# Kernel optimization log

Hardware: AMD Instinct MI355X
Metric: run time of the kernel (lower is better)

## Reference

```python
import jax, jax.numpy as jnp
import numpy as np

N, C_IN, C_OUT, K_CHEB, BATCH = 2048, 64, 64, 4, 8


def setup_inputs() -> dict:
    key = jax.random.key(0)
    k1, k2, k3, k4, k5 = jax.random.split(key, 5)
    # Xavier-uniform-like scales
    s_nn = float(np.sqrt(6.0 / (N + N)))
    s_th = float(np.sqrt(6.0 / (C_IN + C_OUT)))
    return {
        "X": jax.random.normal(k1, (BATCH, N, C_IN), dtype=jnp.float32),
        "Ws": jax.random.uniform(k2, (N, N), jnp.float32, -s_nn, s_nn),
        "W_alpha": jax.random.uniform(k3, (N, N), jnp.float32, -s_nn, s_nn),
        "Theta_s": jax.random.uniform(k4, (K_CHEB, C_IN, C_OUT), jnp.float32, -s_th, s_th),
        "Theta_d": jax.random.uniform(k5, (K_CHEB, C_IN, C_OUT), jnp.float32, -s_th, s_th),
    }


def reference(X, Ws, W_alpha, Theta_s, Theta_d):
    B, n, c_in = X.shape
    K = Theta_s.shape[0]

    # ---- static filter: sum_k (T_k(Ws) @ X) @ Theta_s[k] ----
    # T_0 = I, so T_0 @ X = X
    static_filter = jnp.einsum('bni,io->bno', X, Theta_s[0])
    if K > 1:
        T_prev2 = jnp.eye(n, dtype=X.dtype)
        T_prev1 = Ws  # T_1
        for k in range(1, K):
            TkX = jnp.einsum('nm,bmi->bni', T_prev1, X)
            static_filter = static_filter + jnp.einsum('bni,io->bno', TkX, Theta_s[k])
            if k + 1 < K:  # incremental Chebyshev recursion (same values as from-scratch)
                T_prev2, T_prev1 = T_prev1, 2.0 * (Ws @ T_prev1) - T_prev2

    # ---- dynamic filter ----
    # Wd = X @ (W_alpha @ X)^T  -> [B, n, n]
    WaX = jnp.einsum('nm,bmi->bni', W_alpha, X)
    Wd = jnp.einsum('bni,bmi->bnm', X, WaX)

    dynamic_filter = jnp.einsum('bni,io->bno', X, Theta_d[0])
    if K > 1:
        Td_prev2 = jnp.broadcast_to(jnp.eye(n, dtype=X.dtype), (B, n, n))
        Td_prev1 = Wd  # T_1
        for k in range(1, K):
            TkX = jnp.einsum('bnm,bmi->bni', Td_prev1, X)
            dynamic_filter = dynamic_filter + jnp.einsum('bni,io->bno', TkX, Theta_d[k])
            if k + 1 < K:
                Td_prev2, Td_prev1 = Td_prev1, 2.0 * jnp.matmul(Wd, Td_prev1) - Td_prev2

    return jax.nn.relu(static_filter) + jax.nn.relu(dynamic_filter)
```

## Files before the change

kernel.cpp:

```cpp
#include <hip/hip_runtime.h>

typedef __attribute__((ext_vector_type(8))) short bf16x8;
typedef __attribute__((ext_vector_type(4))) float f32x4;

__device__ __forceinline__ ushort f32_to_bf16(float f) {
    union { float f; unsigned u; } v; v.f = f;
    unsigned b = v.u + 0x7FFF + ((v.u >> 16) & 1);
    return (ushort)(b >> 16);
}
__device__ __forceinline__ float bf16_to_f32(ushort h) {
    union { unsigned u; float f; } v; v.u = ((unsigned)h) << 16;
    return v.f;
}
__device__ __forceinline__ void split2(float x, ushort& a, ushort& b) {
    a = f32_to_bf16(x); float r1 = x - bf16_to_f32(a);
    b = f32_to_bf16(r1);
}

__device__ __forceinline__ void vmwait4() { asm volatile("s_waitcnt vmcnt(4)" ::: "memory"); }
__device__ __forceinline__ void vmwait0() { asm volatile("s_waitcnt vmcnt(0)" ::: "memory"); }
__device__ __forceinline__ void lgwait0() { asm volatile("s_waitcnt lgkmcnt(0)" ::: "memory"); }
__device__ __forceinline__ void blockbar() {
    __builtin_amdgcn_sched_barrier(0);
    __builtin_amdgcn_s_barrier();
    __builtin_amdgcn_sched_barrier(0);
}

__device__ __forceinline__ void stage64x64(const ushort* gsrc, int row_stride_elems,
                                           char* lds, int t256) {
    const char* gb = (const char*)gsrc;
    const int rs = row_stride_elems * 2;
#pragma unroll
    for (int j = 0; j < 2; ++j) {
        int o = (j * 256 + t256) * 16;
        int row = o >> 7;
        int col = (o & 127) ^ ((row & 7) << 4);
        __builtin_amdgcn_global_load_lds(
            (const __attribute__((address_space(1))) unsigned int*)(gb + row * rs + col),
            (__attribute__((address_space(3))) unsigned int*)(lds + o), 16, 0, 0);
    }
}

__device__ __forceinline__ bf16x8 fragld(const char* lds, int row, int kbyte) {
    return *(const bf16x8*)(lds + (row << 7) + (kbyte ^ ((row & 7) << 4)));
}

__global__ __launch_bounds__(256) void prep_all(const float* __restrict__ X,
        ushort* __restrict__ XT1, ushort* __restrict__ XT2,
        ushort* __restrict__ X1o, ushort* __restrict__ X2o,
        const float* __restrict__ Ws, ushort* __restrict__ Ws16,
        const float* __restrict__ Wa, ushort* __restrict__ Wa1, ushort* __restrict__ Wa2,
        const float* __restrict__ Ths, ushort* __restrict__ ThsT) {
    __shared__ float tile[64][68];
    const int bx = blockIdx.x;
    const int t = threadIdx.x;
    if (bx < 256) {
        const int b = bx >> 5, n0 = (bx & 31) * 64;
#pragma unroll
        for (int it = 0; it < 4; ++it) {
            int f = it * 256 + t, r = f >> 4, q = (f & 15) * 4;
            float4 v = *(const float4*)&X[((size_t)b * 2048 + n0 + r) * 64 + q];
            tile[r][q + 0] = v.x; tile[r][q + 1] = v.y; tile[r][q + 2] = v.z; tile[r][q + 3] = v.w;
        }
        __syncthreads();
#pragma unroll
        for (int it = 0; it < 4; ++it) {
            int f = it * 256 + t, c = f >> 4, q = (f & 15) * 4;
            ushort4 h1, h2;
            split2(tile[q + 0][c], h1.x, h2.x); split2(tile[q + 1][c], h1.y, h2.y);
            split2(tile[q + 2][c], h1.z, h2.z); split2(tile[q + 3][c], h1.w, h2.w);
            size_t a = (size_t)(b * 64 + c) * 2048 + n0 + q;
            *(ushort4*)&XT1[a] = h1; *(ushort4*)&XT2[a] = h2;
        }
#pragma unroll
        for (int it = 0; it < 4; ++it) {
            int f = it * 256 + t, n = f >> 4, q = (f & 15) * 4;
            ushort4 h1, h2;
            split2(tile[n][q + 0], h1.x, h2.x); split2(tile[n][q + 1], h1.y, h2.y);
            split2(tile[n][q + 2], h1.z, h2.z); split2(tile[n][q + 3], h1.w, h2.w);
            size_t a = (size_t)(n0 + n) * 512 + b * 64 + q;
            *(ushort4*)&X1o[a] = h1; *(ushort4*)&X2o[a] = h2;
        }
    } else if (bx < 2304) {
        size_t idx = ((size_t)(bx - 256) * 256 + t) * 8;
#pragma unroll
        for (int h = 0; h < 2; ++h) {
            float4 v = *(const float4*)&Ws[idx + h * 4];
            ushort4 a;
            a.x = f32_to_bf16(v.x); a.y = f32_to_bf16(v.y);
            a.z = f32_to_bf16(v.z); a.w = f32_to_bf16(v.w);
            *(ushort4*)&Ws16[idx + h * 4] = a;
        }
    } else if (bx < 4352) {
        size_t idx = ((size_t)(bx - 2304) * 256 + t) * 8;
#pragma unroll
        for (int h = 0; h < 2; ++h) {
            float4 v = *(const float4*)&Wa[idx + h * 4];
            ushort4 a, b;
            split2(v.x, a.x, b.x); split2(v.y, a.y, b.y);
            split2(v.z, a.z, b.z); split2(v.w, a.w, b.w);
            *(ushort4*)&Wa1[idx + h * 4] = a; *(ushort4*)&Wa2[idx + h * 4] = b;
        }
    } else {
        int idx = (bx - 4352) * 256 + t;
        int k = idx >> 12, o = (idx >> 6) & 63, i = idx & 63;
        ThsT[idx] = f32_to_bf16(Ths[k * 4096 + i * 64 + o]);
    }
}

template <int MODE>
__device__ __forceinline__ void gemm_s_body(int bx, const ushort* __restrict__ A,
        const ushort* __restrict__ BT, const ushort* __restrict__ CinT,
        ushort* __restrict__ YT, ushort* __restrict__ Yo, char* ls) {
    const int t = threadIdx.x;
    const int g = t >> 8, t256 = t & 255;
    const int m0 = (bx & 31) * 64, c0 = (bx >> 5) * 64;
    const int lane = t & 63;
    const int wg = (t >> 6) & 3, wr = wg >> 1, wc = wg & 1;
    const int l15 = lane & 15, l4 = lane >> 4;
    char* base = ls + g * 32768;
    const ushort* Ap = A + (size_t)m0 * 2048 + (size_t)g * 1024;
    const ushort* Bp = BT + (size_t)c0 * 2048 + (size_t)g * 1024;

    f32x4 z = {0.f, 0.f, 0.f, 0.f};
    f32x4 acc[2][2];
    acc[0][0] = z; acc[0][1] = z; acc[1][0] = z; acc[1][1] = z;

    stage64x64(Ap, 2048, base, t256);
    stage64x64(Bp, 2048, base + 8192, t256);
    for (int ts = 0; ts < 16; ++ts) {
        char* cur = base + (ts & 1) * 16384;
        if (ts < 15) {
            char* nxt = base + ((ts + 1) & 1) * 16384;
            stage64x64(Ap + (ts + 1) * 64, 2048, nxt, t256);
            stage64x64(Bp + (ts + 1) * 64, 2048, nxt + 8192, t256);
            vmwait4();
        } else {
            vmwait0();
        }
        blockbar();
#pragma unroll
        for (int s = 0; s < 2; ++s) {
            const int kb = s * 64 + l4 * 16;
            bf16x8 aF[2], bF[2];
#pragma unroll
            for (int f = 0; f < 2; ++f) {
                aF[f] = fragld(cur, wr * 32 + f * 16 + l15, kb);
                bF[f] = fragld(cur + 8192, wc * 32 + f * 16 + l15, kb);
            }
#pragma unroll
            for (int i = 0; i < 2; ++i)
#pragma unroll
                for (int j = 0; j < 2; ++j)
                    acc[i][j] = __builtin_amdgcn_mfma_f32_16x16x32_bf16(aF[i], bF[j], acc[i][j], 0, 0, 0);
        }
        lgwait0();
        blockbar();
    }

    float* red = (float*)ls;
    ushort* tileo = (ushort*)(ls + 17408);
    if (g == 0) {
#pragma unroll
        for (int i = 0; i < 2; ++i)
#pragma unroll
            for (int j = 0; j < 2; ++j) {
                const int lrb = wr * 32 + i * 16 + l4 * 4;
                const int lc = wc * 32 + j * 16 + l15;
#pragma unroll
                for (int r = 0; r < 4; ++r) red[(lrb + r) * 65 + lc] = acc[i][j][r];
            }
    }
    __syncthreads();
    if (g == 1) {
#pragma unroll
        for (int i = 0; i < 2; ++i)
#pragma unroll
            for (int j = 0; j < 2; ++j) {
                const int lrb = wr * 32 + i * 16 + l4 * 4;
                const int lc = wc * 32 + j * 16 + l15;
                float vv[4];
#pragma unroll
                for (int r = 0; r < 4; ++r) vv[r] = red[(lrb + r) * 65 + lc] + acc[i][j][r];
                if (MODE == 1) {
                    ushort4 ci = *(const ushort4*)&CinT[(size_t)(c0 + lc) * 2048 + m0 + lrb];
                    vv[0] = 2.f * vv[0] - bf16_to_f32(ci.x);
                    vv[1] = 2.f * vv[1] - bf16_to_f32(ci.y);
                    vv[2] = 2.f * vv[2] - bf16_to_f32(ci.z);
                    vv[3] = 2.f * vv[3] - bf16_to_f32(ci.w);
                }
                ushort4 p;
                p.x = f32_to_bf16(vv[0]); p.y = f32_to_bf16(vv[1]);
                p.z = f32_to_bf16(vv[2]); p.w = f32_to_bf16(vv[3]);
                *(ushort4*)&YT[(size_t)(c0 + lc) * 2048 + m0 + lrb] = p;
                tileo[(lrb + 0) * 64 + lc] = p.x;
                tileo[(lrb + 1) * 64 + lc] = p.y;
                tileo[(lrb + 2) * 64 + lc] = p.z;
                tileo[(lrb + 3) * 64 + lc] = p.w;
            }
    }
    __syncthreads();
    {
        int row = t >> 3, ch = t & 7;
        *(uint4*)&Yo[(size_t)(m0 + row) * 512 + c0 + ch * 8] = *(uint4*)&tileo[row * 64 + ch * 8];
    }
}

__device__ __forceinline__ void gemm3_body(int bx, const ushort* __restrict__ A1,
        const ushort* __restrict__ A2, const ushort* __restrict__ B1,
        const ushort* __restrict__ B2, float* __restrict__ WaXT, char* ls) {
    const int t = threadIdx.x;
    const int g = t >> 8, t256 = t & 255;
    const int m0 = (bx & 31) * 64, c0 = (bx >> 5) * 64;
    const int lane = t & 63;
    const int wg = (t >> 6) & 3, wr = wg >> 1, wc = wg & 1;
    const int l15 = lane & 15, l4 = lane >> 4;
    char* base = ls + g * 32768;
    const size_t kbase = (size_t)g * 1024;

    f32x4 z = {0.f, 0.f, 0.f, 0.f};
    f32x4 acc[2][2];
    acc[0][0] = z; acc[0][1] = z; acc[1][0] = z; acc[1][1] = z;

    for (int k0 = 0; k0 < 1024; k0 += 64) {
        stage64x64(A1 + (size_t)m0 * 2048 + kbase + k0, 2048, base + 0 * 8192, t256);
        stage64x64(A2 + (size_t)m0 * 2048 + kbase + k0, 2048, base + 1 * 8192, t256);
        stage64x64(B1 + (size_t)c0 * 2048 + kbase + k0, 2048, base + 2 * 8192, t256);
        stage64x64(B2 + (size_t)c0 * 2048 + kbase + k0, 2048, base + 3 * 8192, t256);
        __syncthreads();
#pragma unroll
        for (int s = 0; s < 2; ++s) {
            const int kb = s * 64 + l4 * 16;
            bf16x8 a1F[2], a2F[2], b1F[2], b2F[2];
#pragma unroll
            for (int f = 0; f < 2; ++f) {
                const int ar = wr * 32 + f * 16 + l15;
                const int br = wc * 32 + f * 16 + l15;
                a1F[f] = fragld(base + 0 * 8192, ar, kb);
                a2F[f] = fragld(base + 1 * 8192, ar, kb);
                b1F[f] = fragld(base + 2 * 8192, br, kb);
                b2F[f] = fragld(base + 3 * 8192, br, kb);
            }
#pragma unroll
            for (int i = 0; i < 2; ++i)
#pragma unroll
                for (int j = 0; j < 2; ++j) {
                    f32x4 a = acc[i][j];
                    a = __builtin_amdgcn_mfma_f32_16x16x32_bf16(a1F[i], b1F[j], a, 0, 0, 0);
                    a = __builtin_amdgcn_mfma_f32_16x16x32_bf16(a1F[i], b2F[j], a, 0, 0, 0);
                    a = __builtin_amdgcn_mfma_f32_16x16x32_bf16(a2F[i], b1F[j], a, 0, 0, 0);
                    acc[i][j] = a;
                }
        }
        __syncthreads();
    }

    float* red = (float*)ls;
    if (g == 0) {
#pragma unroll
        for (int i = 0; i < 2; ++i)
#pragma unroll
            for (int j = 0; j < 2; ++j) {
                const int lrb = wr * 32 + i * 16 + l4 * 4;
                const int lc = wc * 32 + j * 16 + l15;
#pragma unroll
                for (int r = 0; r < 4; ++r) red[(lrb + r) * 65 + lc] = acc[i][j][r];
            }
    }
    __syncthreads();
    if (g == 1) {
#pragma unroll
        for (int i = 0; i < 2; ++i)
#pragma unroll
            for (int j = 0; j < 2; ++j) {
                const int lrb = wr * 32 + i * 16 + l4 * 4;
                const int lc = wc * 32 + j * 16 + l15;
                f32x4 v;
#pragma unroll
                for (int r = 0; r < 4; ++r) v[r] = red[(lrb + r) * 65 + lc] + acc[i][j][r];
                *(f32x4*)&WaXT[(size_t)(c0 + lc) * 2048 + m0 + lrb] = v;
            }
    }
}

__device__ __forceinline__ void gram_body(int bx, const float* __restrict__ WaXT,
        const ushort* __restrict__ XT1, const ushort* __restrict__ XT2,
        float* __restrict__ Gpart, char* lsraw) {
    const int b = bx & 7, chunk = bx >> 3;
    float (*Lw)[68] = (float(*)[68])lsraw;
    float (*Rx)[68] = (float(*)[68])(lsraw + 64 * 68 * 4);
    const int t = threadIdx.x;
    const int n0 = chunk * 64;
    {
        const int r = t >> 3, q = (t & 7) * 8;
        size_t a = (size_t)(b * 64 + r) * 2048 + n0 + q;
        *(float4*)&Lw[r][q]     = *(const float4*)&WaXT[a];
        *(float4*)&Lw[r][q + 4] = *(const float4*)&WaXT[a + 4];
#pragma unroll
        for (int h = 0; h < 2; ++h) {
            ushort4 h1 = *(const ushort4*)&XT1[a + h * 4];
            ushort4 h2 = *(const ushort4*)&XT2[a + h * 4];
            Rx[r][q + h * 4 + 0] = bf16_to_f32(h1.x) + bf16_to_f32(h2.x);
            Rx[r][q + h * 4 + 1] = bf16_to_f32(h1.y) + bf16_to_f32(h2.y);
            Rx[r][q + h * 4 + 2] = bf16_to_f32(h1.z) + bf16_to_f32(h2.z);
            Rx[r][q + h * 4 + 3] = bf16_to_f32(h1.w) + bf16_to_f32(h2.w);
        }
    }
    __syncthreads();
    if (t < 256) {
        const int tx = t & 15, ty = t >> 4;
        float acc[4][4] = {{0.f,0.f,0.f,0.f},{0.f,0.f,0.f,0.f},{0.f,0.f,0.f,0.f},{0.f,0.f,0.f,0.f}};
        for (int n = 0; n < 64; ++n) {
            float a[4], bb[4];
#pragma unroll
            for (int i = 0; i < 4; ++i) { a[i] = Lw[ty * 4 + i][n]; bb[i] = Rx[tx * 4 + i][n]; }
#pragma unroll
            for (int i = 0; i < 4; ++i)
#pragma unroll
                for (int j = 0; j < 4; ++j) acc[i][j] = fmaf(a[i], bb[j], acc[i][j]);
        }
        float* gp = Gpart + (size_t)(chunk * 8 + b) * 4096;
#pragma unroll
        for (int i = 0; i < 4; ++i)
            *(float4*)&gp[(ty * 4 + i) * 64 + tx * 4] =
                make_float4(acc[i][0], acc[i][1], acc[i][2], acc[i][3]);
    }
}

__device__ __forceinline__ void cheb_body(int b, const float* __restrict__ Gpart,
        const float* __restrict__ Thd, ushort* __restrict__ DT1, ushort* __restrict__ DT2,
        char* lsraw) {
    float (*Gs)[68]  = (float(*)[68])lsraw;
    float (*C2s)[68] = (float(*)[68])(lsraw + 17408);
    float (*C3s)[68] = (float(*)[68])(lsraw + 34816);
    const int t = threadIdx.x;
    for (int i = t; i < 4096; i += 512) {
        float s = 0.f;
#pragma unroll
        for (int c = 0; c < 32; ++c) s += Gpart[((size_t)c * 8 + b) * 4096 + i];
        Gs[i >> 6][i & 63] = s;
    }
    __syncthreads();
    const int tx = t & 15, ty = (t >> 4) & 15;
    const int r0 = ty * 4, c0 = tx * 4;
    const bool act = t < 256;

    if (act) {
        float p[4][4] = {{0,0,0,0},{0,0,0,0},{0,0,0,0},{0,0,0,0}};
        for (int k = 0; k < 64; ++k) {
            float ar[4] = {Gs[r0][k], Gs[r0+1][k], Gs[r0+2][k], Gs[r0+3][k]};
            float4 bv = *(const float4*)&Gs[k][c0];
            float br[4] = {bv.x, bv.y, bv.z, bv.w};
#pragma unroll
            for (int i = 0; i < 4; ++i)
#pragma unroll
                for (int j = 0; j < 4; ++j) p[i][j] = fmaf(ar[i], br[j], p[i][j]);
        }
#pragma unroll
        for (int i = 0; i < 4; ++i)
#pragma unroll
            for (int j = 0; j < 4; ++j)
                C2s[r0+i][c0+j] = 2.f * p[i][j] - ((r0+i) == (c0+j) ? 1.f : 0.f);
    }
    __syncthreads();
    if (act) {
        float q[4][4] = {{0,0,0,0},{0,0,0,0},{0,0,0,0},{0,0,0,0}};
        for (int k = 0; k < 64; ++k) {
            float ar[4] = {Gs[r0][k], Gs[r0+1][k], Gs[r0+2][k], Gs[r0+3][k]};
            float4 bv = *(const float4*)&C2s[k][c0];
            float br[4] = {bv.x, bv.y, bv.z, bv.w};
#pragma unroll
            for (int i = 0; i < 4; ++i)
#pragma unroll
                for (int j = 0; j < 4; ++j) q[i][j] = fmaf(ar[i], br[j], q[i][j]);
        }
#pragma unroll
        for (int i = 0; i < 4; ++i)
#pragma unroll
            for (int j = 0; j < 4; ++j)
                C3s[r0+i][c0+j] = 2.f * q[i][j] - Gs[r0+i][c0+j];
    }
    __syncthreads();
    float d[4][4];
    if (act) {
#pragma unroll
        for (int i = 0; i < 4; ++i) {
            float4 t0 = *(const float4*)&Thd[(r0+i) * 64 + c0];
            d[i][0] = t0.x; d[i][1] = t0.y; d[i][2] = t0.z; d[i][3] = t0.w;
        }
        for (int k = 0; k < 64; ++k) {
            float4 t1 = *(const float4*)&Thd[4096 + k * 64 + c0];
            float4 t2 = *(const float4*)&Thd[8192 + k * 64 + c0];
            float4 t3 = *(const float4*)&Thd[12288 + k * 64 + c0];
            float a1[4] = {Gs[r0][k], Gs[r0+1][k], Gs[r0+2][k], Gs[r0+3][k]};
            float a2[4] = {C2s[r0][k], C2s[r0+1][k], C2s[r0+2][k], C2s[r0+3][k]};
            float a3[4] = {C3s[r0][k], C3s[r0+1][k], C3s[r0+2][k], C3s[r0+3][k]};
            float b1[4] = {t1.x, t1.y, t1.z, t1.w};
            float b2[4] = {t2.x, t2.y, t2.z, t2.w};
            float b3[4] = {t3.x, t3.y, t3.z, t3.w};
#pragma unroll
            for (int i = 0; i < 4; ++i)
#pragma unroll
                for (int j = 0; j < 4; ++j) {
                    d[i][j] = fmaf(a1[i], b1[j], d[i][j]);
                    d[i][j] = fmaf(a2[i], b2[j], d[i][j]);
                    d[i][j] = fmaf(a3[i], b3[j], d[i][j]);
                }
        }
    }
    __syncthreads();
    if (act) {
#pragma unroll
        for (int i = 0; i < 4; ++i)
#pragma unroll
            for (int j = 0; j < 4; ++j) Gs[r0 + i][c0 + j] = d[i][j];
    }
    __syncthreads();
    for (int it = 0; it < 8; ++it) {
        int idx = it * 512 + t;
        int o = idx >> 6, ii = idx & 63;
        ushort h1, h2;
        split2(Gs[ii][o], h1, h2);
        DT1[b * 4096 + idx] = h1;
        DT2[b * 4096 + idx] = h2;
    }
}

__global__ __launch_bounds__(512, 4) void mega1(const ushort* __restrict__ Wa1,
        const ushort* __restrict__ Wa2, const ushort* __restrict__ XT1,
        const ushort* __restrict__ XT2, float* __restrict__ WaXT,
        const ushort* __restrict__ Ws16, ushort* __restrict__ Y1T, ushort* __restrict__ Y1o) {
    __shared__ __align__(16) char ls[65536];
    const int bx = blockIdx.x;
    if (bx < 256) gemm3_body(bx, Wa1, Wa2, XT1, XT2, WaXT, ls);
    else          gemm_s_body<0>(bx - 256, Ws16, XT1, nullptr, Y1T, Y1o, ls);
}

__global__ __launch_bounds__(512, 4) void mega2(const ushort* __restrict__ Ws16,
        const ushort* __restrict__ Y1T, const ushort* __restrict__ XT1,
        ushort* __restrict__ Y2T, ushort* __restrict__ Y2o,
        const float* __restrict__ WaXT, const ushort* __restrict__ XT2,
        float* __restrict__ Gpart) {
    __shared__ __align__(16) char ls[65536];
    const int bx = blockIdx.x;
    if (bx < 256) gemm_s_body<1>(bx, Ws16, Y1T, XT1, Y2T, Y2o, ls);
    else          gram_body(bx - 256, WaXT, XT1, XT2, Gpart, ls);
}

__global__ __launch_bounds__(512, 4) void mega3(const ushort* __restrict__ Ws16,
        const ushort* __restrict__ Y2T, const ushort* __restrict__ Y1T,
        ushort* __restrict__ Y3T, ushort* __restrict__ Y3o,
        const float* __restrict__ Gpart, const float* __restrict__ Thd,
        ushort* __restrict__ DT1, ushort* __restrict__ DT2) {
    __shared__ __align__(16) char ls[65536];
    const int bx = blockIdx.x;
    if (bx < 256) gemm_s_body<1>(bx, Ws16, Y2T, Y1T, Y3T, Y3o, ls);
    else          cheb_body(bx - 256, Gpart, Thd, DT1, DT2, ls);
}

__global__ __launch_bounds__(256) void ep_fused(const ushort* __restrict__ ThsT,
                                                const ushort* __restrict__ DT1, const ushort* __restrict__ DT2,
                                                const ushort* __restrict__ X1o, const ushort* __restrict__ X2o,
                                                const ushort* __restrict__ Y1o, const ushort* __restrict__ Y2o,
                                                const ushort* __restrict__ Y3o,
                                                float* __restrict__ out) {
    __shared__ __align__(16) char ls[65536];
    const int b = blockIdx.y, n0 = blockIdx.x * 64;
    const int t = threadIdx.x, lane = t & 63, w = t >> 6, wr = w >> 1, wc = w & 1;
    const int l15 = lane & 15, l4 = lane >> 4;
    stage64x64(X1o + (size_t)n0 * 512 + b * 64, 512, ls + 0 * 8192, t);
    stage64x64(Y1o + (size_t)n0 * 512 + b * 64, 512, ls + 1 * 8192, t);
    stage64x64(Y2o + (size_t)n0 * 512 + b * 64, 512, ls + 2 * 8192, t);
    stage64x64(Y3o + (size_t)n0 * 512 + b * 64, 512, ls + 3 * 8192, t);
    stage64x64(ThsT + 0 * 4096, 64, ls + 4 * 8192, t);
    stage64x64(ThsT + 1 * 4096, 64, ls + 5 * 8192, t);
    stage64x64(ThsT + 2 * 4096, 64, ls + 6 * 8192, t);
    stage64x64(ThsT + 3 * 4096, 64, ls + 7 * 8192, t);
    __syncthreads();
    f32x4 z = {0.f, 0.f, 0.f, 0.f};
    f32x4 as[2][2], ad[2][2];
    as[0][0] = z; as[0][1] = z; as[1][0] = z; as[1][1] = z;
    ad[0][0] = z; ad[0][1] = z; ad[1][0] = z; ad[1][1] = z;
#pragma unroll
    for (int s = 0; s < 2; ++s) {
        const int kb = s * 64 + l4 * 16;
#pragma unroll
        for (int p = 0; p < 4; ++p) {
            bf16x8 aF[2], bF[2];
#pragma unroll
            for (int f = 0; f < 2; ++f) {
                aF[f] = fragld(ls + (4 + p) * 8192, wr * 32 + f * 16 + l15, kb);
                bF[f] = fragld(ls + p * 8192, wc * 32 + f * 16 + l15, kb);
            }
#pragma unroll
            for (int i = 0; i < 2; ++i)
#pragma unroll
                for (int j = 0; j < 2; ++j)
                    as[i][j] = __builtin_amdgcn_mfma_f32_16x16x32_bf16(aF[i], bF[j], as[i][j], 0, 0, 0);
        }
    }
    __syncthreads();
    stage64x64(DT1 + b * 4096, 64, ls + 1 * 8192, t);
    stage64x64(DT2 + b * 4096, 64, ls + 2 * 8192, t);
    stage64x64(X2o + (size_t)n0 * 512 + b * 64, 512, ls + 3 * 8192, t);
    __syncthreads();
#pragma unroll
    for (int s = 0; s < 2; ++s) {
        const int kb = s * 64 + l4 * 16;
        bf16x8 a1[2], a2[2], b0[2], b3[2];
#pragma unroll
        for (int f = 0; f < 2; ++f) {
            a1[f] = fragld(ls + 1 * 8192, wr * 32 + f * 16 + l15, kb);
            a2[f] = fragld(ls + 2 * 8192, wr * 32 + f * 16 + l15, kb);
            b0[f] = fragld(ls + 0 * 8192, wc * 32 + f * 16 + l15, kb);
            b3[f] = fragld(ls + 3 * 8192, wc * 32 + f * 16 + l15, kb);
        }
#pragma unroll
        for (int i = 0; i < 2; ++i)
#pragma unroll
            for (int j = 0; j < 2; ++j) {
                f32x4 a = ad[i][j];
                a = __builtin_amdgcn_mfma_f32_16x16x32_bf16(a1[i], b0[j], a, 0, 0, 0);
                a = __builtin_amdgcn_mfma_f32_16x16x32_bf16(a1[i], b3[j], a, 0, 0, 0);
                a = __builtin_amdgcn_mfma_f32_16x16x32_bf16(a2[i], b0[j], a, 0, 0, 0);
                ad[i][j] = a;
            }
    }
#pragma unroll
    for (int i = 0; i < 2; ++i)
#pragma unroll
        for (int j = 0; j < 2; ++j) {
            const int ob = wr * 32 + i * 16 + l4 * 4;
            const int nn = wc * 32 + j * 16 + l15;
            float4 o4;
            o4.x = fmaxf(as[i][j][0], 0.f) + fmaxf(ad[i][j][0], 0.f);
            o4.y = fmaxf(as[i][j][1], 0.f) + fmaxf(ad[i][j][1], 0.f);
            o4.z = fmaxf(as[i][j][2], 0.f) + fmaxf(ad[i][j][2], 0.f);
            o4.w = fmaxf(as[i][j][3], 0.f) + fmaxf(ad[i][j][3], 0.f);
            *(float4*)&out[((size_t)b * 2048 + n0 + nn) * 64 + ob] = o4;
        }
}

extern "C" void kernel_launch(void* const* d_in, const int* in_sizes, int n_in,
                              void* d_out, int out_size, void* d_ws, size_t ws_size,
                              hipStream_t stream) {
    (void)in_sizes; (void)n_in; (void)out_size;
    const float* X   = (const float*)d_in[0];
    const float* Ws  = (const float*)d_in[1];
    const float* Wa  = (const float*)d_in[2];
    const float* Ths = (const float*)d_in[3];
    const float* Thd = (const float*)d_in[4];

    char* p = (char*)d_ws;
    auto alloc = [&](size_t bytes) { char* r = p; p += (bytes + 255) & ~(size_t)255; return r; };
    ushort* XT1 = (ushort*)alloc(512ull * 2048 * 2);
    ushort* XT2 = (ushort*)alloc(512ull * 2048 * 2);
    ushort* X1o = (ushort*)alloc(2048ull * 512 * 2);
    ushort* X2o = (ushort*)alloc(2048ull * 512 * 2);
    ushort* Ws16 = (ushort*)alloc(2048ull * 2048 * 2);
    ushort* Wa1 = (ushort*)alloc(2048ull * 2048 * 2);
    ushort* Wa2 = (ushort*)alloc(2048ull * 2048 * 2);
    ushort* Y1T = (ushort*)alloc(512ull * 2048 * 2);
    ushort* Y2T = (ushort*)alloc(512ull * 2048 * 2);
    ushort* Y3T = (ushort*)alloc(512ull * 2048 * 2);
    ushort* Y1o = (ushort*)alloc(2048ull * 512 * 2);
    ushort* Y2o = (ushort*)alloc(2048ull * 512 * 2);
    ushort* Y3o = (ushort*)alloc(2048ull * 512 * 2);
    float*  Gpart = (float*)alloc(32ull * 8 * 4096 * 4);
    ushort* DT1 = (ushort*)alloc(8ull * 4096 * 2);
    ushort* DT2 = (ushort*)alloc(8ull * 4096 * 2);
    ushort* ThsT = (ushort*)alloc(4ull * 4096 * 2);
    if ((size_t)(p - (char*)d_ws) > ws_size) return;
    float* WaXT = (float*)d_out;

    prep_all<<<4416, 256, 0, stream>>>(X, XT1, XT2, X1o, X2o, Ws, Ws16, Wa, Wa1, Wa2, Ths, ThsT);
    mega1<<<512, 512, 0, stream>>>(Wa1, Wa2, XT1, XT2, WaXT, Ws16, Y1T, Y1o);
    mega2<<<512, 512, 0, stream>>>(Ws16, Y1T, XT1, Y2T, Y2o, WaXT, XT2, Gpart);
    mega3<<<264, 512, 0, stream>>>(Ws16, Y2T, Y1T, Y3T, Y3o, Gpart, Thd, DT1, DT2);
    ep_fused<<<dim3(32, 8), 256, 0, stream>>>(ThsT, DT1, DT2, X1o, X2o, Y1o, Y2o, Y3o, (float*)d_out);
}
```

Measured before the change: 88.71 us.

## Split Y3 GEMM into split-K partials and fuse Chebyshev combine into epilogue

The third static Chebyshev GEMM (Ws @ Y2) is split along K into two halves across twice as many blocks. Each block double-buffers its 64x64 tiles and reduces the two in-block K groups through LDS, then writes fp32 partials P0/P1. The epilogue kernel adds the partials, applies 2*P - Y1 and converts to bf16 straight into its LDS tile. This drops the Y3T/Y3o bf16 outputs and spreads the final GEMM over more CUs. The cost is more fp32 partial traffic between the two kernels.

After: 90.97 us. 2.6% more time.

```diff
diff --git a/kernel.cpp b/kernel.cpp
--- a/kernel.cpp
+++ b/kernel.cpp
@@ -206,6 +206,91 @@
     }
 }
 
+__device__ __forceinline__ void y3_body(int bx, const ushort* __restrict__ A,
+        const ushort* __restrict__ BT, float* __restrict__ P0, float* __restrict__ P1,
+        char* ls) {
+    const int t = threadIdx.x;
+    const int g = t >> 8, t256 = t & 255;
+    const int tile = bx >> 1, g2 = bx & 1;
+    const int m0 = (tile & 31) * 64, c0 = (tile >> 5) * 64;
+    const int lane = t & 63;
+    const int wg = (t >> 6) & 3, wr = wg >> 1, wc = wg & 1;
+    const int l15 = lane & 15, l4 = lane >> 4;
+    char* base = ls + g * 32768;
+    const size_t kbase = (size_t)g2 * 1024 + (size_t)g * 512;
+    const ushort* Ap = A + (size_t)m0 * 2048 + kbase;
+    const ushort* Bp = BT + (size_t)c0 * 2048 + kbase;
+
+    f32x4 z = {0.f, 0.f, 0.f, 0.f};
+    f32x4 acc[2][2];
+    acc[0][0] = z; acc[0][1] = z; acc[1][0] = z; acc[1][1] = z;
+
+    stage64x64(Ap, 2048, base, t256);
+    stage64x64(Bp, 2048, base + 8192, t256);
+    for (int ts = 0; ts < 8; ++ts) {
+        char* cur = base + (ts & 1) * 16384;
+        if (ts < 7) {
+            char* nxt = base + ((ts + 1) & 1) * 16384;
+            stage64x64(Ap + (ts + 1) * 64, 2048, nxt, t256);
+            stage64x64(Bp + (ts + 1) * 64, 2048, nxt + 8192, t256);
+            vmwait4();
+        } else {
+            vmwait0();
+        }
+        blockbar();
+#pragma unroll
+        for (int s = 0; s < 2; ++s) {
+            const int kb = s * 64 + l4 * 16;
+            bf16x8 aF[2], bF[2];
+#pragma unroll
+            for (int f = 0; f < 2; ++f) {
+                aF[f] = fragld(cur, wr * 32 + f * 16 + l15, kb);
+                bF[f] = fragld(cur + 8192, wc * 32 + f * 16 + l15, kb);
+            }
+#pragma unroll
+            for (int i = 0; i < 2; ++i)
+#pragma unroll
+                for (int j = 0; j < 2; ++j)
+                    acc[i][j] = __builtin_amdgcn_mfma_f32_16x16x32_bf16(aF[i], bF[j], acc[i][j], 0, 0, 0);
+        }
+        lgwait0();
+        blockbar();
+    }
+
+    float* red = (float*)ls;
+    float* tf = (float*)(ls + 17408);
+    if (g == 0) {
+#pragma unroll
+        for (int i = 0; i < 2; ++i)
+#pragma unroll
+            for (int j = 0; j < 2; ++j) {
+                const int lrb = wr * 32 + i * 16 + l4 * 4;
+                const int lc = wc * 32 + j * 16 + l15;
+#pragma unroll
+                for (int r = 0; r < 4; ++r) red[(lrb + r) * 65 + lc] = acc[i][j][r];
+            }
+    }
+    __syncthreads();
+    if (g == 1) {
+#pragma unroll
+        for (int i = 0; i < 2; ++i)
+#pragma unroll
+            for (int j = 0; j < 2; ++j) {
+                const int lrb = wr * 32 + i * 16 + l4 * 4;
+                const int lc = wc * 32 + j * 16 + l15;
+#pragma unroll
+                for (int r = 0; r < 4; ++r) tf[(lrb + r) * 64 + lc] = red[(lrb + r) * 65 + lc] + acc[i][j][r];
+            }
+    }
+    __syncthreads();
+    {
+        float* Pd = g2 ? P1 : P0;
+        int row = t >> 3, q = (t & 7) * 8;
+        *(float4*)&Pd[(size_t)(m0 + row) * 512 + c0 + q]     = *(float4*)&tf[row * 64 + q];
+        *(float4*)&Pd[(size_t)(m0 + row) * 512 + c0 + q + 4] = *(float4*)&tf[row * 64 + q + 4];
+    }
+}
+
 __device__ __forceinline__ void gemm3_body(int bx, const ushort* __restrict__ A1,
         const ushort* __restrict__ A2, const ushort* __restrict__ B1,
         const ushort* __restrict__ B2, float* __restrict__ WaXT, char* ls) {
@@ -448,35 +533,73 @@
 }
 
 __global__ __launch_bounds__(512, 4) void mega3(const ushort* __restrict__ Ws16,
-        const ushort* __restrict__ Y2T, const ushort* __restrict__ Y1T,
-        ushort* __restrict__ Y3T, ushort* __restrict__ Y3o,
+        const ushort* __restrict__ Y2T, float* __restrict__ P0, float* __restrict__ P1,
         const float* __restrict__ Gpart, const float* __restrict__ Thd,
         ushort* __restrict__ DT1, ushort* __restrict__ DT2) {
     __shared__ __align__(16) char ls[65536];
     const int bx = blockIdx.x;
-    if (bx < 256) gemm_s_body<1>(bx, Ws16, Y2T, Y1T, Y3T, Y3o, ls);
-    else          cheb_body(bx - 256, Gpart, Thd, DT1, DT2, ls);
+    if (bx < 512) y3_body(bx, Ws16, Y2T, P0, P1, ls);
+    else          cheb_body(bx - 512, Gpart, Thd, DT1, DT2, ls);
 }
 
 __global__ __launch_bounds__(256) void ep_fused(const ushort* __restrict__ ThsT,
                                                 const ushort* __restrict__ DT1, const ushort* __restrict__ DT2,
                                                 const ushort* __restrict__ X1o, const ushort* __restrict__ X2o,
                                                 const ushort* __restrict__ Y1o, const ushort* __restrict__ Y2o,
-                                                const ushort* __restrict__ Y3o,
+                                                const float* __restrict__ P0, const float* __restrict__ P1,
                                                 float* __restrict__ out) {
     __shared__ __align__(16) char ls[65536];
     const int b = blockIdx.y, n0 = blockIdx.x * 64;
     const int t = threadIdx.x, lane = t & 63, w = t >> 6, wr = w >> 1, wc = w & 1;
     const int l15 = lane & 15, l4 = lane >> 4;
+
+    const int r3 = t >> 2, q3e = (t & 3) * 16;
+    const size_t a3 = (size_t)(n0 + r3) * 512 + b * 64 + q3e;
+    float4 pA[4], pB[4];
+    ushort4 y1v[4];
+#pragma unroll
+    for (int h = 0; h < 4; ++h) {
+        pA[h]  = *(const float4*)&P0[a3 + h * 4];
+        pB[h]  = *(const float4*)&P1[a3 + h * 4];
+        y1v[h] = *(const ushort4*)&Y1o[a3 + h * 4];
+    }
+
     stage64x64(X1o + (size_t)n0 * 512 + b * 64, 512, ls + 0 * 8192, t);
     stage64x64(Y1o + (size_t)n0 * 512 + b * 64, 512, ls + 1 * 8192, t);
     stage64x64(Y2o + (size_t)n0 * 512 + b * 64, 512, ls + 2 * 8192, t);
-    stage64x64(Y3o + (size_t)n0 * 512 + b * 64, 512, ls + 3 * 8192, t);
     stage64x64(ThsT + 0 * 4096, 64, ls + 4 * 8192, t);
     stage64x64(ThsT + 1 * 4096, 64, ls + 5 * 8192, t);
     stage64x64(ThsT + 2 * 4096, 64, ls + 6 * 8192, t);
     stage64x64(ThsT + 3 * 4096, 64, ls + 7 * 8192, t);
-    __syncthreads();
+    {
+        uint4 w0, w1;
+        ushort* u0 = (ushort*)&w0;
+        ushort* u1 = (ushort*)&w1;
+#pragma unroll
+        for (int h = 0; h < 2; ++h) {
+            const float4 pa = pA[h], pb = pB[h];
+            const ushort4 yv = y1v[h];
+            u0[h * 4 + 0] = f32_to_bf16(2.f * (pa.x + pb.x) - bf16_to_f32(yv.x));
+            u0[h * 4 + 1] = f32_to_bf16(2.f * (pa.y + pb.y) - bf16_to_f32(yv.y));
+            u0[h * 4 + 2] = f32_to_bf16(2.f * (pa.z + pb.z) - bf16_to_f32(yv.z));
+            u0[h * 4 + 3] = f32_to_bf16(2.f * (pa.w + pb.w) - bf16_to_f32(yv.w));
+        }
+#pragma unroll
+        for (int h = 0; h < 2; ++h) {
+            const float4 pa = pA[2 + h], pb = pB[2 + h];
+            const ushort4 yv = y1v[2 + h];
+            u1[h * 4 + 0] = f32_to_bf16(2.f * (pa.x + pb.x) - bf16_to_f32(yv.x));
+            u1[h * 4 + 1] = f32_to_bf16(2.f * (pa.y + pb.y) - bf16_to_f32(yv.y));
+            u1[h * 4 + 2] = f32_to_bf16(2.f * (pa.z + pb.z) - bf16_to_f32(yv.z));
+            u1[h * 4 + 3] = f32_to_bf16(2.f * (pa.w + pb.w) - bf16_to_f32(yv.w));
+        }
+        const int bc0 = q3e * 2;
+        const int sw = (r3 & 7) << 4;
+        *(uint4*)(ls + 3 * 8192 + (r3 << 7) + ((bc0 + 0)  ^ sw)) = w0;
+        *(uint4*)(ls + 3 * 8192 + (r3 << 7) + ((bc0 + 16) ^ sw)) = w1;
+    }
+    __syncthreads();
+
     f32x4 z = {0.f, 0.f, 0.f, 0.f};
     f32x4 as[2][2], ad[2][2];
     as[0][0] = z; as[0][1] = z; as[1][0] = z; as[1][1] = z;
@@ -562,10 +685,10 @@
     ushort* Wa2 = (ushort*)alloc(2048ull * 2048 * 2);
     ushort* Y1T = (ushort*)alloc(512ull * 2048 * 2);
     ushort* Y2T = (ushort*)alloc(512ull * 2048 * 2);
-    ushort* Y3T = (ushort*)alloc(512ull * 2048 * 2);
     ushort* Y1o = (ushort*)alloc(2048ull * 512 * 2);
     ushort* Y2o = (ushort*)alloc(2048ull * 512 * 2);
-    ushort* Y3o = (ushort*)alloc(2048ull * 512 * 2);
+    float*  P0  = (float*)alloc(2048ull * 512 * 4);
+    float*  P1  = (float*)alloc(2048ull * 512 * 4);
     float*  Gpart = (float*)alloc(32ull * 8 * 4096 * 4);
     ushort* DT1 = (ushort*)alloc(8ull * 4096 * 2);
     ushort* DT2 = (ushort*)alloc(8ull * 4096 * 2);
@@ -576,6 +699,6 @@
     prep_all<<<4416, 256, 0, stream>>>(X, XT1, XT2, X1o, X2o, Ws, Ws16, Wa, Wa1, Wa2, Ths, ThsT);
     mega1<<<512, 512, 0, stream>>>(Wa1, Wa2, XT1, XT2, WaXT, Ws16, Y1T, Y1o);
     mega2<<<512, 512, 0, stream>>>(Ws16, Y1T, XT1, Y2T, Y2o, WaXT, XT2, Gpart);
-    mega3<<<264, 512, 0, stream>>>(Ws16, Y2T, Y1T, Y3T, Y3o, Gpart, Thd, DT1, DT2);
-    ep_fused<<<dim3(32, 8), 256, 0, stream>>>(ThsT, DT1, DT2, X1o, X2o, Y1o, Y2o, Y3o, (float*)d_out);
-}
+    mega3<<<520, 512, 0, stream>>>(Ws16, Y2T, P0, P1, Gpart, Thd, DT1, DT2);
+    ep_fused<<<dim3(32, 8), 256, 0, stream>>>(ThsT, DT1, DT2, X1o, X2o, Y1o, Y2o, P0, P1, (float*)d_out);
+}
```
